# Kernel tuning notes

Measured on AMD Instinct MI355X. Metric: run time of the kernel, lower is better.

## Reference

```python
import jax, jax.numpy as jnp
import numpy as np

B, V, F, P, E = 4, 8192, 16384, 4, 2048


def setup_inputs() -> dict:
    key = jax.random.key(0)
    k1, k2, k3, k4, k5 = jax.random.split(key, 5)
    xs = jax.random.normal(k1, (B, V, 3), dtype=jnp.float32)
    y = jax.random.normal(k2, (B, V, 3), dtype=jnp.float32)
    # projection matrices [P,3,4]; make the 3rd (homogeneous-divide) row
    # close to [0,0,0,1] so projected depth ~1 and the divide is stable.
    pm = jax.random.normal(k3, (P, 3, 4), dtype=jnp.float32)
    pm = pm.at[:, 2, :].set(jnp.asarray([0.0, 0.0, 0.0, 1.0], jnp.float32)
                            + 0.01 * jax.random.normal(k5, (P, 4), dtype=jnp.float32))
    edgemaps = jax.random.normal(k4, (B, P, E, 2), dtype=jnp.float32)
    faces = jax.random.randint(jax.random.fold_in(key, 7), (B, F, 3), 0, V, dtype=jnp.int32)
    return {"xs": xs, "y": y, "projmatrices": pm, "edgemaps": edgemaps, "faces": faces}


def _volumes(verts, faces):
    fv = jax.vmap(lambda v, f: v[f])(verts, faces)        # [B,F,3,3]
    v0, v1, v2 = fv[:, :, 0], fv[:, :, 1], fv[:, :, 2]
    face_vol = jnp.sum(jnp.cross(v0, v1) * v2, axis=-1) / 6.0  # [B,F]
    return jnp.abs(jnp.sum(face_vol, axis=-1))                 # [B]


def reference(xs, y, projmatrices, edgemaps, faces):
    lambda_proj, lambda_vol = 1.0, 1.0
    # ---- lsq_proj: per-mesh SSE between original and projected verts ----
    lsq = jnp.sum(jnp.square(xs - y), axis=(-1, -2))            # [B]
    # ---- volume constraint (target volume is a fixed buffer from src) ----
    target_vol = jax.lax.stop_gradient(_volumes(xs, faces))
    vol_loss = jnp.square(_volumes(y, faces) - target_vol)      # [B]
    # ---- silhouette chamfer: project verts into P views, chamfer vs edgemaps
    ones = jnp.ones((B, V, 1), dtype=y.dtype)
    y_h = jnp.concatenate([y, ones], axis=-1)                   # [B,V,4]
    proj = jnp.einsum('pij,bvj->bpvi', projmatrices, y_h)       # [B,P,V,3]
    pts = proj[..., :2] / proj[..., 2:3]                        # [B,P,V,2]
    # pairwise squared distances [B,P,V,E]
    d2 = jnp.sum(jnp.square(pts[:, :, :, None, :] - edgemaps[:, :, None, :, :]), axis=-1)
    cham_x = jnp.mean(jnp.min(d2, axis=3), axis=2)              # [B,P] boundary->edgemap
    cham_y = jnp.mean(jnp.min(d2, axis=2), axis=2)              # [B,P] edgemap->boundary
    chamfer = jnp.mean(cham_x + cham_y, axis=1)                 # [B] batch_reduction='mean' over views
    return chamfer + lambda_proj * lsq + lambda_vol * vol_loss
```

## Files before the change

### kernel.cpp

```cpp
#include <hip/hip_runtime.h>

#define B 4
#define V 8192
#define F 16384
#define P 4
#define E 2048
#define NPAIR 16

#define WS_PTS   0
#define WS_ER    524288
#define WS_VMIN  655360
#define WS_EMIN  786432
#define WS_LSQP  819200
#define WS_VOLPX 819328
#define WS_VOLPY 819584
#define WS_CX    819840
#define WS_CY    819856

#define INFBITS 0x7F800000u

__device__ __forceinline__ float block_sum(float v, float* sred) {
    #pragma unroll
    for (int off = 32; off; off >>= 1) v += __shfl_down(v, off, 64);
    int w = threadIdx.x >> 6, l = threadIdx.x & 63;
    if (l == 0) sred[w] = v;
    __syncthreads();
    float r = 0.f;
    if (threadIdx.x == 0) {
        r = sred[0];
        for (int i = 1; i < ((int)blockDim.x >> 6); ++i) r += sred[i];
    }
    __syncthreads();
    return r;
}

__device__ __forceinline__ float facevol(const float* __restrict__ vb,
                                         int i0, int i1, int i2) {
    float a0 = vb[i0 * 3], a1 = vb[i0 * 3 + 1], a2 = vb[i0 * 3 + 2];
    float b0 = vb[i1 * 3], b1 = vb[i1 * 3 + 1], b2 = vb[i1 * 3 + 2];
    float c0 = vb[i2 * 3], c1 = vb[i2 * 3 + 1], c2 = vb[i2 * 3 + 2];
    float cx = a1 * b2 - a2 * b1;
    float cy = a2 * b0 - a0 * b2;
    float cz = a0 * b1 - a1 * b0;
    return (cx * c0 + cy * c1 + cz * c2) * (1.0f / 6.0f);
}

__global__ void __launch_bounds__(256) k_pre(const float* __restrict__ xs,
                                             const float* __restrict__ y,
                                             const float* __restrict__ pm,
                                             const float* __restrict__ em,
                                             const int* __restrict__ faces,
                                             float* __restrict__ ws) {
    __shared__ float spm[48];
    __shared__ float sred[4];
    int tid = threadIdx.x;
    int blk = blockIdx.x;

    if (blk < 128) {
        if (tid < 48) spm[tid] = pm[tid];
        __syncthreads();
        int b = blk >> 5;
        int v = ((blk & 31) << 8) + tid;
        size_t base = ((size_t)b * V + v) * 3;
        float y0 = y[base], y1 = y[base + 1], y2 = y[base + 2];
        float x0 = xs[base], x1 = xs[base + 1], x2 = xs[base + 2];
        float d0 = x0 - y0, d1 = x1 - y1, d2 = x2 - y2;
        float lsq = d0 * d0 + d1 * d1 + d2 * d2;

        float4* pts = (float4*)(ws + WS_PTS);
        #pragma unroll
        for (int p = 0; p < P; ++p) {
            const float* m = spm + p * 12;
            float xw = m[0] * y0 + m[1] * y1 + m[2]  * y2 + m[3];
            float yw = m[4] * y0 + m[5] * y1 + m[6]  * y2 + m[7];
            float w  = m[8] * y0 + m[9] * y1 + m[10] * y2 + m[11];
            float px = xw / w, py = yw / w;
            pts[(size_t)(b * P + p) * V + v] = make_float4(px, py, px * px + py * py, 0.f);
        }
        float s = block_sum(lsq, sred);
        if (tid == 0) ws[WS_LSQP + blk] = s;
    } else if (blk < 384) {
        int blk2 = blk - 128;
        int b = blk2 >> 6;
        int f = ((blk2 & 63) << 8) + tid;
        size_t fb = ((size_t)b * F + f) * 3;
        int i0 = faces[fb], i1 = faces[fb + 1], i2 = faces[fb + 2];
        const float* xb = xs + (size_t)b * V * 3;
        const float* yb = y  + (size_t)b * V * 3;
        float sx = block_sum(facevol(xb, i0, i1, i2), sred);
        float sy = block_sum(facevol(yb, i0, i1, i2), sred);
        if (tid == 0) { ws[WS_VOLPX + blk2] = sx; ws[WS_VOLPY + blk2] = sy; }
    } else {
        int i = (blk - 384) * 256 + tid;
        ((unsigned*)(ws + WS_VMIN))[i] = INFBITS;
        if (i < NPAIR * E) {
            ((unsigned*)(ws + WS_EMIN))[i] = INFBITS;
            float2 e = ((const float2*)em)[i];
            ((float4*)(ws + WS_ER))[i] = make_float4(e.x, e.y, e.x * e.x + e.y * e.y, 0.f);
        }
        if (i < 32) ws[WS_CX + i] = 0.f;
    }
}

__global__ void __launch_bounds__(256) k_cham(float* __restrict__ ws) {
    __shared__ float4 sbuf[256];
    int tid = threadIdx.x;
    int blk = blockIdx.x;

    if (blk < 512) {
        int pair = blk >> 5;
        int vch = (blk >> 3) & 3;
        int ech = blk & 7;
        sbuf[tid] = ((const float4*)(ws + WS_ER))[(size_t)pair * E + ech * 256 + tid];

        const float4* pts = (const float4*)(ws + WS_PTS) + (size_t)pair * V + vch * 2048 + tid;
        float px2[8], py2[8], pz[8], mn[8];
        #pragma unroll
        for (int k = 0; k < 8; ++k) {
            float4 p = pts[k * 256];
            px2[k] = -2.f * p.x; py2[k] = -2.f * p.y; pz[k] = p.z;
            mn[k] = 3.4e38f;
        }
        __syncthreads();
        #pragma unroll 4
        for (int i = 0; i < 256; ++i) {
            float4 e = sbuf[i];
            #pragma unroll
            for (int k = 0; k < 8; ++k)
                mn[k] = fminf(mn[k], fmaf(px2[k], e.x, fmaf(py2[k], e.y, e.z)));
        }
        unsigned* vmin = (unsigned*)(ws + WS_VMIN) + (size_t)pair * V + vch * 2048 + tid;
        #pragma unroll
        for (int k = 0; k < 8; ++k)
            atomicMin(vmin + k * 256, __float_as_uint(mn[k] + pz[k]));
    } else {
        int blk2 = blk - 512;
        int pair = blk2 >> 5;
        int vch = blk2 & 31;
        sbuf[tid] = ((const float4*)(ws + WS_PTS))[(size_t)pair * V + vch * 256 + tid];

        const float4* er = (const float4*)(ws + WS_ER) + (size_t)pair * E + tid;
        float ex2[8], ey2[8], ez[8], mn[8];
        #pragma unroll
        for (int k = 0; k < 8; ++k) {
            float4 e = er[k * 256];
            ex2[k] = -2.f * e.x; ey2[k] = -2.f * e.y; ez[k] = e.z;
            mn[k] = 3.4e38f;
        }
        __syncthreads();
        #pragma unroll 4
        for (int i = 0; i < 256; ++i) {
            float4 p = sbuf[i];
            #pragma unroll
            for (int k = 0; k < 8; ++k)
                mn[k] = fminf(mn[k], fmaf(ex2[k], p.x, fmaf(ey2[k], p.y, p.z)));
        }
        unsigned* emin = (unsigned*)(ws + WS_EMIN) + (size_t)pair * E + tid;
        #pragma unroll
        for (int k = 0; k < 8; ++k)
            atomicMin(emin + k * 256, __float_as_uint(mn[k] + ez[k]));
    }
}

__global__ void __launch_bounds__(256) k_red(float* __restrict__ ws) {
    __shared__ float sred[4];
    int tid = threadIdx.x;
    int blk = blockIdx.x;
    float val;
    float* dst;
    if (blk < 512) {
        int idx = blk * 256 + tid;
        val = ws[WS_VMIN + idx] * (1.0f / V);
        dst = ws + WS_CX + (blk >> 5);
    } else {
        int idx = (blk - 512) * 256 + tid;
        val = ws[WS_EMIN + idx] * (1.0f / E);
        dst = ws + WS_CY + ((blk - 512) >> 3);
    }
    float s = block_sum(val, sred);
    if (tid == 0) atomicAdd(dst, s);
}

__global__ void __launch_bounds__(256) k_out(float* __restrict__ ws,
                                             float* __restrict__ out) {
    __shared__ float sred[4];
    int tid = threadIdx.x;
    int b = blockIdx.x;
    float c = (tid < P) ? (ws[WS_CX + b * P + tid] + ws[WS_CY + b * P + tid]) : 0.f;
    float cham = block_sum(c, sred);
    float volx = block_sum((tid < 64) ? ws[WS_VOLPX + b * 64 + tid] : 0.f, sred);
    float voly = block_sum((tid < 64) ? ws[WS_VOLPY + b * 64 + tid] : 0.f, sred);
    float lsq  = block_sum((tid < 32) ? ws[WS_LSQP  + b * 32 + tid] : 0.f, sred);
    if (tid == 0) {
        float dv = fabsf(voly) - fabsf(volx);
        out[b] = cham * (1.0f / P) + lsq + dv * dv;
    }
}

extern "C" void kernel_launch(void* const* d_in, const int* in_sizes, int n_in,
                              void* d_out, int out_size, void* d_ws, size_t ws_size,
                              hipStream_t stream) {
    const float* xs    = (const float*)d_in[0];
    const float* y     = (const float*)d_in[1];
    const float* pm    = (const float*)d_in[2];
    const float* em    = (const float*)d_in[3];
    const int*   faces = (const int*)d_in[4];
    float* ws  = (float*)d_ws;
    float* out = (float*)d_out;

    hipLaunchKernelGGL(k_pre,  dim3(896),  dim3(256), 0, stream, xs, y, pm, em, faces, ws);
    hipLaunchKernelGGL(k_cham, dim3(1024), dim3(256), 0, stream, ws);
    hipLaunchKernelGGL(k_red,  dim3(640),  dim3(256), 0, stream, ws);
    hipLaunchKernelGGL(k_out,  dim3(4),    dim3(256), 0, stream, ws, out);
}
```

Baseline: 110.1 us.

## Compute each distance tile once and derive both row and column minima

The chamfer kernel previously evaluated the full point-to-edge distance matrix twice, once per direction. It now has each block tile 256 vertices against all 2048 edge points held in LDS. Each distance feeds both a per-vertex minimum (shuffle reduction plus LDS atomics) and a per-edge minimum (register accumulators plus global atomics), which halves the arithmetic. The -2 scaling is moved into the preprocessing stage. In exchange the block uses more LDS, holds 32 accumulators per thread and issues more global atomics for the edge minima.

```diff
diff --git a/kernel.cpp b/kernel.cpp
--- a/kernel.cpp
+++ b/kernel.cpp
@@ -6,6 +6,8 @@
 #define P 4
 #define E 2048
 #define NPAIR 16
+
+typedef float f32x4 __attribute__((ext_vector_type(4)));
 
 #define WS_PTS   0
 #define WS_ER    524288
@@ -75,7 +77,8 @@
             float yw = m[4] * y0 + m[5] * y1 + m[6]  * y2 + m[7];
             float w  = m[8] * y0 + m[9] * y1 + m[10] * y2 + m[11];
             float px = xw / w, py = yw / w;
-            pts[(size_t)(b * P + p) * V + v] = make_float4(px, py, px * px + py * py, 0.f);
+            pts[(size_t)(b * P + p) * V + v] =
+                make_float4(-2.f * px, -2.f * py, px * px + py * py, 0.f);
         }
         float s = block_sum(lsq, sred);
         if (tid == 0) ws[WS_LSQP + blk] = s;
@@ -96,70 +99,83 @@
         if (i < NPAIR * E) {
             ((unsigned*)(ws + WS_EMIN))[i] = INFBITS;
             float2 e = ((const float2*)em)[i];
-            ((float4*)(ws + WS_ER))[i] = make_float4(e.x, e.y, e.x * e.x + e.y * e.y, 0.f);
+            ((float4*)(ws + WS_ER))[i] =
+                make_float4(e.x, e.y, e.x * e.x + e.y * e.y, 0.f);
         }
         if (i < 32) ws[WS_CX + i] = 0.f;
     }
 }
 
 __global__ void __launch_bounds__(256) k_cham(float* __restrict__ ws) {
-    __shared__ float4 sbuf[256];
+    __shared__ float4 s_eb[E];
+    __shared__ float4 s_pb[256];
+    __shared__ unsigned s_rmin[256];
     int tid = threadIdx.x;
     int blk = blockIdx.x;
-
-    if (blk < 512) {
-        int pair = blk >> 5;
-        int vch = (blk >> 3) & 3;
-        int ech = blk & 7;
-        sbuf[tid] = ((const float4*)(ws + WS_ER))[(size_t)pair * E + ech * 256 + tid];
-
-        const float4* pts = (const float4*)(ws + WS_PTS) + (size_t)pair * V + vch * 2048 + tid;
-        float px2[8], py2[8], pz[8], mn[8];
+    int pair = blk >> 5;
+    int vblk = blk & 31;
+
+    const float4* ebg = (const float4*)(ws + WS_ER) + (size_t)pair * E;
+    #pragma unroll
+    for (int i = 0; i < 8; ++i) s_eb[tid + i * 256] = ebg[tid + i * 256];
+    s_pb[tid] = ((const float4*)(ws + WS_PTS))[(size_t)pair * V + vblk * 256 + tid];
+    s_rmin[tid] = INFBITS;
+    __syncthreads();
+
+    int lane = tid & 63, wv = tid >> 6;
+    int c = lane & 15, g = lane >> 4;
+    int eoff = wv * 512;
+
+    float colacc[32];
+    #pragma unroll
+    for (int t = 0; t < 32; ++t) colacc[t] = 3.4e38f;
+
+    for (int vt = 0; vt < 16; ++vt) {
+        float4 p0 = s_pb[vt * 16 + g * 4 + 0];
+        float4 p1 = s_pb[vt * 16 + g * 4 + 1];
+        float4 p2 = s_pb[vt * 16 + g * 4 + 2];
+        float4 p3 = s_pb[vt * 16 + g * 4 + 3];
+
+        f32x4 racc = {3.4e38f, 3.4e38f, 3.4e38f, 3.4e38f};
         #pragma unroll
-        for (int k = 0; k < 8; ++k) {
-            float4 p = pts[k * 256];
-            px2[k] = -2.f * p.x; py2[k] = -2.f * p.y; pz[k] = p.z;
-            mn[k] = 3.4e38f;
-        }
-        __syncthreads();
-        #pragma unroll 4
-        for (int i = 0; i < 256; ++i) {
-            float4 e = sbuf[i];
-            #pragma unroll
-            for (int k = 0; k < 8; ++k)
-                mn[k] = fminf(mn[k], fmaf(px2[k], e.x, fmaf(py2[k], e.y, e.z)));
-        }
-        unsigned* vmin = (unsigned*)(ws + WS_VMIN) + (size_t)pair * V + vch * 2048 + tid;
+        for (int t = 0; t < 32; ++t) {
+            float4 ev = s_eb[eoff + t * 16 + c];
+            float d0 = fmaf(p0.x, ev.x, fmaf(p0.y, ev.y, p0.z + ev.z));
+            float d1 = fmaf(p1.x, ev.x, fmaf(p1.y, ev.y, p1.z + ev.z));
+            float d2 = fmaf(p2.x, ev.x, fmaf(p2.y, ev.y, p2.z + ev.z));
+            float d3 = fmaf(p3.x, ev.x, fmaf(p3.y, ev.y, p3.z + ev.z));
+            racc[0] = fminf(racc[0], d0);
+            racc[1] = fminf(racc[1], d1);
+            racc[2] = fminf(racc[2], d2);
+            racc[3] = fminf(racc[3], d3);
+            colacc[t] = fminf(colacc[t], fminf(fminf(d0, d1), fminf(d2, d3)));
+        }
         #pragma unroll
-        for (int k = 0; k < 8; ++k)
-            atomicMin(vmin + k * 256, __float_as_uint(mn[k] + pz[k]));
-    } else {
-        int blk2 = blk - 512;
-        int pair = blk2 >> 5;
-        int vch = blk2 & 31;
-        sbuf[tid] = ((const float4*)(ws + WS_PTS))[(size_t)pair * V + vch * 256 + tid];
-
-        const float4* er = (const float4*)(ws + WS_ER) + (size_t)pair * E + tid;
-        float ex2[8], ey2[8], ez[8], mn[8];
-        #pragma unroll
-        for (int k = 0; k < 8; ++k) {
-            float4 e = er[k * 256];
-            ex2[k] = -2.f * e.x; ey2[k] = -2.f * e.y; ez[k] = e.z;
-            mn[k] = 3.4e38f;
-        }
-        __syncthreads();
-        #pragma unroll 4
-        for (int i = 0; i < 256; ++i) {
-            float4 p = sbuf[i];
-            #pragma unroll
-            for (int k = 0; k < 8; ++k)
-                mn[k] = fminf(mn[k], fmaf(ex2[k], p.x, fmaf(ey2[k], p.y, p.z)));
-        }
-        unsigned* emin = (unsigned*)(ws + WS_EMIN) + (size_t)pair * E + tid;
-        #pragma unroll
-        for (int k = 0; k < 8; ++k)
-            atomicMin(emin + k * 256, __float_as_uint(mn[k] + ez[k]));
-    }
+        for (int off = 1; off <= 8; off <<= 1) {
+            racc[0] = fminf(racc[0], __shfl_xor(racc[0], off, 64));
+            racc[1] = fminf(racc[1], __shfl_xor(racc[1], off, 64));
+            racc[2] = fminf(racc[2], __shfl_xor(racc[2], off, 64));
+            racc[3] = fminf(racc[3], __shfl_xor(racc[3], off, 64));
+        }
+        if (c == 0) {
+            atomicMin(&s_rmin[vt * 16 + g * 4 + 0], __float_as_uint(racc[0]));
+            atomicMin(&s_rmin[vt * 16 + g * 4 + 1], __float_as_uint(racc[1]));
+            atomicMin(&s_rmin[vt * 16 + g * 4 + 2], __float_as_uint(racc[2]));
+            atomicMin(&s_rmin[vt * 16 + g * 4 + 3], __float_as_uint(racc[3]));
+        }
+    }
+
+    unsigned* emin = (unsigned*)(ws + WS_EMIN) + (size_t)pair * E + eoff;
+    #pragma unroll
+    for (int t = 0; t < 32; ++t) {
+        float v = colacc[t];
+        v = fminf(v, __shfl_xor(v, 16, 64));
+        v = fminf(v, __shfl_xor(v, 32, 64));
+        if (lane < 16) atomicMin(emin + t * 16 + c, __float_as_uint(v));
+    }
+    __syncthreads();
+    atomicMin((unsigned*)(ws + WS_VMIN) + (size_t)pair * V + vblk * 256 + tid,
+              s_rmin[tid]);
 }
 
 __global__ void __launch_bounds__(256) k_red(float* __restrict__ ws) {
@@ -208,8 +224,8 @@
     float* ws  = (float*)d_ws;
     float* out = (float*)d_out;
 
-    hipLaunchKernelGGL(k_pre,  dim3(896),  dim3(256), 0, stream, xs, y, pm, em, faces, ws);
-    hipLaunchKernelGGL(k_cham, dim3(1024), dim3(256), 0, stream, ws);
-    hipLaunchKernelGGL(k_red,  dim3(640),  dim3(256), 0, stream, ws);
-    hipLaunchKernelGGL(k_out,  dim3(4),    dim3(256), 0, stream, ws, out);
-}
+    hipLaunchKernelGGL(k_pre,  dim3(896), dim3(256), 0, stream, xs, y, pm, em, faces, ws);
+    hipLaunchKernelGGL(k_cham, dim3(512), dim3(256), 0, stream, ws);
+    hipLaunchKernelGGL(k_red,  dim3(640), dim3(256), 0, stream, ws);
+    hipLaunchKernelGGL(k_out,  dim3(4),   dim3(256), 0, stream, ws, out);
+}
```

New measurement: 128.6 us. 1.17x slower.

## Replace chamfer atomicMin with per-chunk partial minima reduced in second pass

Applied to the files above, without the earlier changes.

The chamfer kernel now writes per-chunk partial minima to separate workspace slices instead of doing atomicMin into shared min arrays, and the reduce kernel takes the min across slices before summing. The tiles are halved to 128 points each, so twice as many blocks launch. The -2 scale on points is folded into preprocessing, and the infinity initialisation of the min buffers is removed. This trades contended atomics and an init pass for extra workspace traffic (16 and 64 partial slices) and more blocks.

```diff
diff --git a/kernel.cpp b/kernel.cpp
--- a/kernel.cpp
+++ b/kernel.cpp
@@ -9,15 +9,13 @@
 
 #define WS_PTS   0
 #define WS_ER    524288
-#define WS_VMIN  655360
-#define WS_EMIN  786432
-#define WS_LSQP  819200
-#define WS_VOLPX 819328
-#define WS_VOLPY 819584
-#define WS_CX    819840
-#define WS_CY    819856
-
-#define INFBITS 0x7F800000u
+#define WS_VP    655360
+#define WS_EP    2752512
+#define WS_LSQP  4849664
+#define WS_VOLPX 4849792
+#define WS_VOLPY 4850048
+#define WS_CX    4850304
+#define WS_CY    4850320
 
 __device__ __forceinline__ float block_sum(float v, float* sred) {
     #pragma unroll
@@ -75,7 +73,8 @@
             float yw = m[4] * y0 + m[5] * y1 + m[6]  * y2 + m[7];
             float w  = m[8] * y0 + m[9] * y1 + m[10] * y2 + m[11];
             float px = xw / w, py = yw / w;
-            pts[(size_t)(b * P + p) * V + v] = make_float4(px, py, px * px + py * py, 0.f);
+            pts[(size_t)(b * P + p) * V + v] =
+                make_float4(-2.f * px, -2.f * py, px * px + py * py, 0.f);
         }
         float s = block_sum(lsq, sred);
         if (tid == 0) ws[WS_LSQP + blk] = s;
@@ -92,73 +91,72 @@
         if (tid == 0) { ws[WS_VOLPX + blk2] = sx; ws[WS_VOLPY + blk2] = sy; }
     } else {
         int i = (blk - 384) * 256 + tid;
-        ((unsigned*)(ws + WS_VMIN))[i] = INFBITS;
-        if (i < NPAIR * E) {
-            ((unsigned*)(ws + WS_EMIN))[i] = INFBITS;
-            float2 e = ((const float2*)em)[i];
-            ((float4*)(ws + WS_ER))[i] = make_float4(e.x, e.y, e.x * e.x + e.y * e.y, 0.f);
-        }
-        if (i < 32) ws[WS_CX + i] = 0.f;
+        float2 e = ((const float2*)em)[i];
+        ((float4*)(ws + WS_ER))[i] =
+            make_float4(e.x, e.y, e.x * e.x + e.y * e.y, 0.f);
+        if (blk == 384 && tid < 32) ws[WS_CX + tid] = 0.f;
     }
 }
 
 __global__ void __launch_bounds__(256) k_cham(float* __restrict__ ws) {
-    __shared__ float4 sbuf[256];
+    __shared__ float4 sbuf[128];
     int tid = threadIdx.x;
     int blk = blockIdx.x;
 
-    if (blk < 512) {
-        int pair = blk >> 5;
-        int vch = (blk >> 3) & 3;
-        int ech = blk & 7;
-        sbuf[tid] = ((const float4*)(ws + WS_ER))[(size_t)pair * E + ech * 256 + tid];
+    if (blk < 1024) {
+        int pair = blk >> 6;
+        int vch = (blk >> 4) & 3;
+        int ech = blk & 15;
+        if (tid < 128)
+            sbuf[tid] = ((const float4*)(ws + WS_ER))[(size_t)pair * E + ech * 128 + tid];
 
         const float4* pts = (const float4*)(ws + WS_PTS) + (size_t)pair * V + vch * 2048 + tid;
         float px2[8], py2[8], pz[8], mn[8];
         #pragma unroll
         for (int k = 0; k < 8; ++k) {
             float4 p = pts[k * 256];
-            px2[k] = -2.f * p.x; py2[k] = -2.f * p.y; pz[k] = p.z;
+            px2[k] = p.x; py2[k] = p.y; pz[k] = p.z;
             mn[k] = 3.4e38f;
         }
         __syncthreads();
         #pragma unroll 4
-        for (int i = 0; i < 256; ++i) {
+        for (int i = 0; i < 128; ++i) {
             float4 e = sbuf[i];
             #pragma unroll
             for (int k = 0; k < 8; ++k)
                 mn[k] = fminf(mn[k], fmaf(px2[k], e.x, fmaf(py2[k], e.y, e.z)));
         }
-        unsigned* vmin = (unsigned*)(ws + WS_VMIN) + (size_t)pair * V + vch * 2048 + tid;
+        float* vp = ws + WS_VP + (size_t)ech * (NPAIR * V) + (size_t)pair * V + vch * 2048 + tid;
         #pragma unroll
         for (int k = 0; k < 8; ++k)
-            atomicMin(vmin + k * 256, __float_as_uint(mn[k] + pz[k]));
+            vp[k * 256] = mn[k] + pz[k];
     } else {
-        int blk2 = blk - 512;
-        int pair = blk2 >> 5;
-        int vch = blk2 & 31;
-        sbuf[tid] = ((const float4*)(ws + WS_PTS))[(size_t)pair * V + vch * 256 + tid];
+        int blk2 = blk - 1024;
+        int pair = blk2 >> 6;
+        int vch = blk2 & 63;
+        if (tid < 128)
+            sbuf[tid] = ((const float4*)(ws + WS_PTS))[(size_t)pair * V + vch * 128 + tid];
 
         const float4* er = (const float4*)(ws + WS_ER) + (size_t)pair * E + tid;
-        float ex2[8], ey2[8], ez[8], mn[8];
+        float ex[8], ey[8], ez[8], mn[8];
         #pragma unroll
         for (int k = 0; k < 8; ++k) {
             float4 e = er[k * 256];
-            ex2[k] = -2.f * e.x; ey2[k] = -2.f * e.y; ez[k] = e.z;
+            ex[k] = e.x; ey[k] = e.y; ez[k] = e.z;
             mn[k] = 3.4e38f;
         }
         __syncthreads();
         #pragma unroll 4
-        for (int i = 0; i < 256; ++i) {
+        for (int i = 0; i < 128; ++i) {
             float4 p = sbuf[i];
             #pragma unroll
             for (int k = 0; k < 8; ++k)
-                mn[k] = fminf(mn[k], fmaf(ex2[k], p.x, fmaf(ey2[k], p.y, p.z)));
-        }
-        unsigned* emin = (unsigned*)(ws + WS_EMIN) + (size_t)pair * E + tid;
+                mn[k] = fminf(mn[k], fmaf(ex[k], p.x, fmaf(ey[k], p.y, p.z)));
+        }
+        float* ep = ws + WS_EP + (size_t)vch * (NPAIR * E) + (size_t)pair * E + tid;
         #pragma unroll
         for (int k = 0; k < 8; ++k)
-            atomicMin(emin + k * 256, __float_as_uint(mn[k] + ez[k]));
+            ep[k * 256] = mn[k] + ez[k];
     }
 }
 
@@ -169,13 +167,24 @@
     float val;
     float* dst;
     if (blk < 512) {
-        int idx = blk * 256 + tid;
-        val = ws[WS_VMIN + idx] * (1.0f / V);
-        dst = ws + WS_CX + (blk >> 5);
+        int pair = blk >> 5;
+        int vidx = (blk & 31) * 256 + tid;
+        const float* vp = ws + WS_VP + (size_t)pair * V + vidx;
+        float m = vp[0];
+        #pragma unroll
+        for (int s = 1; s < 16; ++s) m = fminf(m, vp[(size_t)s * (NPAIR * V)]);
+        val = m * (1.0f / V);
+        dst = ws + WS_CX + pair;
     } else {
-        int idx = (blk - 512) * 256 + tid;
-        val = ws[WS_EMIN + idx] * (1.0f / E);
-        dst = ws + WS_CY + ((blk - 512) >> 3);
+        int blk2 = blk - 512;
+        int pair = blk2 >> 3;
+        int eidx = (blk2 & 7) * 256 + tid;
+        const float* ep = ws + WS_EP + (size_t)pair * E + eidx;
+        float m = ep[0];
+        #pragma unroll
+        for (int s = 1; s < 64; ++s) m = fminf(m, ep[(size_t)s * (NPAIR * E)]);
+        val = m * (1.0f / E);
+        dst = ws + WS_CY + pair;
     }
     float s = block_sum(val, sred);
     if (tid == 0) atomicAdd(dst, s);
@@ -208,8 +217,8 @@
     float* ws  = (float*)d_ws;
     float* out = (float*)d_out;
 
-    hipLaunchKernelGGL(k_pre,  dim3(896),  dim3(256), 0, stream, xs, y, pm, em, faces, ws);
-    hipLaunchKernelGGL(k_cham, dim3(1024), dim3(256), 0, stream, ws);
+    hipLaunchKernelGGL(k_pre,  dim3(512),  dim3(256), 0, stream, xs, y, pm, em, faces, ws);
+    hipLaunchKernelGGL(k_cham, dim3(2048), dim3(256), 0, stream, ws);
     hipLaunchKernelGGL(k_red,  dim3(640),  dim3(256), 0, stream, ws);
     hipLaunchKernelGGL(k_out,  dim3(4),    dim3(256), 0, stream, ws, out);
 }
```

Result: slower. 113.2 us (+2.8%).
